# Kernel tuning notes

Hardware: AMD Instinct MI355X
Metric: run time of the kernel (lower is better)

## Reference

```python
import jax, jax.numpy as jnp
import numpy as np

B, T, N_EMBD, HEAD = 4, 2048, 1024, 128


def setup_inputs() -> dict:
    key = jax.random.key(0)
    ks = jax.random.split(key, 7)
    s = 1.0 / np.sqrt(N_EMBD)
    return {
        "X": jax.random.normal(ks[0], (B, T, N_EMBD), dtype=jnp.float32),
        "Wk": jax.random.normal(ks[1], (N_EMBD, HEAD), dtype=jnp.float32) * s,
        "bk": jax.random.normal(ks[2], (HEAD,), dtype=jnp.float32) * 0.02,
        "Wq": jax.random.normal(ks[3], (N_EMBD, HEAD), dtype=jnp.float32) * s,
        "bq": jax.random.normal(ks[4], (HEAD,), dtype=jnp.float32) * 0.02,
        "Wv": jax.random.normal(ks[5], (N_EMBD, HEAD), dtype=jnp.float32) * s,
        "bv": jax.random.normal(ks[6], (HEAD,), dtype=jnp.float32) * 0.02,
    }


def reference(X, Wk, bk, Wq, bq, Wv, bv):
    # X: [B, T, C] with C = n_embd
    C = X.shape[-1]
    k = X @ Wk + bk  # [B, T, H]
    q = X @ Wq + bq  # [B, T, H]
    # NOTE: original computes k @ q^T (not q @ k^T) and scales by n_embd**-0.5.
    wei = jnp.einsum("bth,bsh->bts", k, q) * (C ** -0.5)  # [B, T, T]
    # NOTE: original's masked_fill is not in-place and its result is discarded,
    # so NO causal mask is actually applied. Dropout is identity (eval).
    wei = jax.nn.softmax(wei, axis=-1)
    v = X @ Wv + bv  # [B, T, H]
    out = jnp.einsum("bts,bsh->bth", wei, v)  # [B, T, H]
    return out
```

## Files before the change

kernel.cpp:

```cpp
#include <hip/hip_runtime.h>
#include <hip/hip_bf16.h>

#define Bn 4
#define Tn 2048
#define Cn 1024
#define Hn 128
#define Mn (Bn*Tn)
#define SCHUNKS 8
#define SCHUNK  (Tn/SCHUNKS)

typedef _Float16 f16;
typedef __attribute__((ext_vector_type(4))) _Float16 f16x4;
typedef __attribute__((ext_vector_type(8))) _Float16 f16x8;
typedef __attribute__((ext_vector_type(4))) float f32x4;

__global__ void prep_w(const float* __restrict__ Wk, const float* __restrict__ Wq,
                       const float* __restrict__ Wv, f16* __restrict__ Wt) {
    const int w = blockIdx.y;
    const float* W = (w == 0) ? Wk : (w == 1) ? Wq : Wv;
    int idx = blockIdx.x * 256 + threadIdx.x;
    int c = idx >> 7;
    int h = idx & 127;
    Wt[w * (Cn * Hn) + h * Cn + c] = (f16)W[idx];
}

__global__ __launch_bounds__(512) void qkv_gemm(const float* __restrict__ X,
                                                const f16* __restrict__ Wt,
                                                const float* __restrict__ bk,
                                                const float* __restrict__ bq,
                                                const float* __restrict__ bv,
                                                f16* __restrict__ proj) {
    __shared__ __align__(16) f16 As[32 * 72];
    __shared__ __align__(16) f16 Bs[384 * 72];

    const int tid  = threadIdx.x;
    const int r0   = blockIdx.x * 32;
    const int lane = tid & 63, wid = tid >> 6;
    const int quad = lane >> 4, l16 = lane & 15;
    const int nbase = wid * 48;

    f32x4 acc[2][3] = {};

    for (int k0 = 0; k0 < Cn; k0 += 64) {
        {
            int row = tid >> 4, c4 = tid & 15;
            float4 x = *(const float4*)(X + (r0 + row) * Cn + k0 + c4 * 4);
            f16x4 v = { (f16)x.x, (f16)x.y, (f16)x.z, (f16)x.w };
            *(f16x4*)(&As[row * 72 + c4 * 4]) = v;
        }
        for (int i = 0; i < 6; i++) {
            int ci = tid + 512 * i;
            int row = ci >> 3, cc = ci & 7;
            *(f16x8*)(&Bs[row * 72 + cc * 8]) =
                *(const f16x8*)(Wt + row * Cn + k0 + cc * 8);
        }
        __syncthreads();
        for (int ks = 0; ks < 2; ks++) {
            int kk = ks * 32;
            f16x8 af[2], bf[3];
            for (int mt = 0; mt < 2; mt++)
                af[mt] = *(const f16x8*)(&As[(mt * 16 + l16) * 72 + kk + quad * 8]);
            for (int nt = 0; nt < 3; nt++)
                bf[nt] = *(const f16x8*)(&Bs[(nbase + nt * 16 + l16) * 72 + kk + quad * 8]);
            for (int mt = 0; mt < 2; mt++)
                for (int nt = 0; nt < 3; nt++)
                    acc[mt][nt] = __builtin_amdgcn_mfma_f32_16x16x32_f16(
                        af[mt], bf[nt], acc[mt][nt], 0, 0, 0);
        }
        __syncthreads();
    }

    for (int nt = 0; nt < 3; nt++) {
        int n0 = nbase + nt * 16;
        int wsel = n0 >> 7;
        int col = (n0 & 127) + l16;
        const float* bias = (wsel == 0) ? bk : (wsel == 1) ? bq : bv;
        float bval = bias[col];
        float scale = (wsel == 0) ? 0.03125f : 1.0f;
        f16* P = proj + wsel * (Mn * Hn);
        for (int mt = 0; mt < 2; mt++)
            for (int r = 0; r < 4; r++) {
                int m = r0 + mt * 16 + quad * 4 + r;
                P[m * Hn + col] = (f16)((acc[mt][nt][r] + bval) * scale);
            }
    }
}

__global__ __launch_bounds__(256) void vt_transpose(const f16* __restrict__ pv,
                                                    f16* __restrict__ vT) {
    __shared__ __align__(16) f16 T[64 * 72];
    const int tid = threadIdx.x;
    const int s0 = blockIdx.x * 64, h0 = blockIdx.y * 64, b = blockIdx.z;
    for (int i = 0; i < 2; i++) {
        int ci = tid + 256 * i;
        int row = ci >> 3, hc = ci & 7;
        *(f16x8*)(&T[row * 72 + hc * 8]) =
            *(const f16x8*)(pv + (b * Tn + s0 + row) * Hn + h0 + hc * 8);
    }
    __syncthreads();
    for (int i = 0; i < 2; i++) {
        int ci = tid + 256 * i;
        int h = ci >> 3, sc = ci & 7;
        f16x8 v;
        for (int j = 0; j < 8; j++) v[j] = T[(sc * 8 + j) * 72 + h];
        *(f16x8*)(&vT[(b * Hn + h0 + h) * Tn + s0 + sc * 8]) = v;
    }
}

__global__ __launch_bounds__(256, 2) void attn_kernel(const f16* __restrict__ pk,
                                                      const f16* __restrict__ pq,
                                                      const f16* __restrict__ vT,
                                                      f16* __restrict__ pO,
                                                      float* __restrict__ pm,
                                                      float* __restrict__ pl) {
    __shared__ __align__(16) char smem[36864];
    f16* Bq = (f16*)smem;
    f16* Vt = (f16*)(smem + 17408);

    const int tid  = threadIdx.x;
    const int tblk = blockIdx.x, c = blockIdx.y, b = blockIdx.z;
    const int t0   = tblk * 128;
    const int lane = tid & 63, wid = tid >> 6;
    const int quad = lane >> 4, l16 = lane & 15;
    const int tw   = t0 + wid * 32;

    const f16* kp = pk + b * Tn * Hn;
    const f16* qp = pq + b * Tn * Hn;
    const f16* vp = vT + b * Hn * Tn;

    f16x8 kfr[2][4];
    for (int tt = 0; tt < 2; tt++)
        for (int ks = 0; ks < 4; ks++)
            kfr[tt][ks] = *(const f16x8*)(kp + (tw + tt * 16 + l16) * Hn + ks * 32 + quad * 8);

    float m_i[2] = { -3e38f, -3e38f }, l_i[2] = { 0.0f, 0.0f };
    f32x4 accO[2][8] = {};

    for (int si = 0; si < SCHUNK / 64; si++) {
        const int s0 = c * SCHUNK + si * 64;
        for (int i = 0; i < 4; i++) {
            int ci = tid + 256 * i;
            int row = ci >> 4, hc = ci & 15;
            *(f16x8*)(&Bq[row * 136 + hc * 8]) =
                *(const f16x8*)(qp + (s0 + row) * Hn + hc * 8);
        }
        for (int i = 0; i < 4; i++) {
            int ci = tid + 256 * i;
            int h = ci >> 3, sc = ci & 7;
            *(f16x8*)(&Vt[h * 72 + sc * 8]) =
                *(const f16x8*)(vp + h * Tn + s0 + sc * 8);
        }
        __syncthreads();

        f32x4 accS[2][4] = {};
        for (int ks = 0; ks < 4; ks++) {
            int kk = ks * 32;
            for (int st = 0; st < 4; st++) {
                f16x8 af = *(const f16x8*)(&Bq[(st * 16 + l16) * 136 + kk + quad * 8]);
                accS[0][st] = __builtin_amdgcn_mfma_f32_16x16x32_f16(af, kfr[0][ks], accS[0][st], 0, 0, 0);
                accS[1][st] = __builtin_amdgcn_mfma_f32_16x16x32_f16(af, kfr[1][ks], accS[1][st], 0, 0, 0);
            }
        }

        f16x4 pf[2][4];
        for (int tt = 0; tt < 2; tt++) {
            float mloc = -3e38f;
            for (int st = 0; st < 4; st++)
                for (int r = 0; r < 4; r++) mloc = fmaxf(mloc, accS[tt][st][r]);
            mloc = fmaxf(mloc, __shfl_xor(mloc, 16));
            mloc = fmaxf(mloc, __shfl_xor(mloc, 32));
            float mnew = fmaxf(m_i[tt], mloc);
            float alpha = __expf(m_i[tt] - mnew);
            m_i[tt] = mnew;
            float psum = 0.0f;
            for (int st = 0; st < 4; st++) {
                f32x4 p;
                for (int r = 0; r < 4; r++) {
                    p[r] = __expf(accS[tt][st][r] - mnew);
                    psum += p[r];
                }
                pf[tt][st] = { (f16)p[0], (f16)p[1], (f16)p[2], (f16)p[3] };
            }
            psum += __shfl_xor(psum, 16);
            psum += __shfl_xor(psum, 32);
            l_i[tt] = l_i[tt] * alpha + psum;
            for (int ht = 0; ht < 8; ht++)
                for (int r = 0; r < 4; r++) accO[tt][ht][r] *= alpha;
        }

        for (int st = 0; st < 4; st++) {
            for (int ht = 0; ht < 8; ht++) {
                f16x4 av = *(const f16x4*)(&Vt[(ht * 16 + l16) * 72 + st * 16 + quad * 4]);
                accO[0][ht] = __builtin_amdgcn_mfma_f32_16x16x16f16(av, pf[0][st], accO[0][ht], 0, 0, 0);
                accO[1][ht] = __builtin_amdgcn_mfma_f32_16x16x16f16(av, pf[1][st], accO[1][ht], 0, 0, 0);
            }
        }
        __syncthreads();
    }

    for (int tt = 0; tt < 2; tt++) {
        __syncthreads();
        float* ep = (float*)smem + wid * 2048;
        for (int ht = 0; ht < 8; ht++)
            for (int r = 0; r < 4; r++)
                ep[(ht * 16 + quad * 4 + r) * 16 + l16] = accO[tt][ht][r];
        __syncthreads();
        {
            int t = lane >> 2, hq = lane & 3;
            int tgl = tw + tt * 16 + t;
            f16* dst = pO + ((size_t)(c * Bn + b) * Tn + tgl) * Hn + hq * 32;
            for (int g = 0; g < 4; g++) {
                f16x8 v;
                for (int j = 0; j < 8; j++)
                    v[j] = (f16)ep[(hq * 32 + g * 8 + j) * 16 + t];
                *(f16x8*)(dst + g * 8) = v;
            }
        }
        if (quad == 0) {
            pm[(c * Bn + b) * Tn + tw + tt * 16 + l16] = m_i[tt];
            pl[(c * Bn + b) * Tn + tw + tt * 16 + l16] = l_i[tt];
        }
    }
}

__global__ __launch_bounds__(256) void merge_kernel(const f16* __restrict__ pO,
                                                    const float* __restrict__ pm,
                                                    const float* __restrict__ pl,
                                                    float* __restrict__ out) {
    int gid = blockIdx.x * 256 + threadIdx.x;
    int tg = gid >> 2;
    int hq = gid & 3;
    float mc[SCHUNKS], lc[SCHUNKS];
    float M = -3e38f;
    for (int cI = 0; cI < SCHUNKS; cI++) {
        mc[cI] = pm[cI * (Bn * Tn) + tg];
        lc[cI] = pl[cI * (Bn * Tn) + tg];
        M = fmaxf(M, mc[cI]);
    }
    float L = 0.0f, wc[SCHUNKS];
    for (int cI = 0; cI < SCHUNKS; cI++) {
        wc[cI] = __expf(mc[cI] - M);
        L += wc[cI] * lc[cI];
    }
    float inv = 1.0f / L;
    float o[32] = {};
    for (int cI = 0; cI < SCHUNKS; cI++) {
        const f16* src = pO + ((size_t)cI * Bn * Tn + tg) * Hn + hq * 32;
        float w = wc[cI];
        for (int g = 0; g < 4; g++) {
            f16x8 v = *(const f16x8*)(src + g * 8);
            for (int j = 0; j < 8; j++) o[g * 8 + j] += w * (float)v[j];
        }
    }
    float* dst = out + (size_t)tg * Hn + hq * 32;
    for (int g = 0; g < 8; g++) {
        float4 v = { o[g*4+0] * inv, o[g*4+1] * inv, o[g*4+2] * inv, o[g*4+3] * inv };
        *(float4*)(dst + g * 4) = v;
    }
}

extern "C" void kernel_launch(void* const* d_in, const int* in_sizes, int n_in,
                              void* d_out, int out_size, void* d_ws, size_t ws_size,
                              hipStream_t stream) {
    const float* X  = (const float*)d_in[0];
    const float* Wk = (const float*)d_in[1];
    const float* bk = (const float*)d_in[2];
    const float* Wq = (const float*)d_in[3];
    const float* bq = (const float*)d_in[4];
    const float* Wv = (const float*)d_in[5];
    const float* bv = (const float*)d_in[6];
    float* out = (float*)d_out;

    char* base = (char*)d_ws;
    f16*   Wt   = (f16*)(base);
    f16*   proj = (f16*)(base + 786432);
    f16*   pk   = proj;
    f16*   pq   = proj + Mn * Hn;
    f16*   pv   = proj + 2 * Mn * Hn;
    f16*   vT   = (f16*)(base + 7077888);
    f16*   pO   = (f16*)(base + 9175040);
    float* pm   = (float*)(base + 25952256);
    float* pl   = (float*)(base + 26214400);

    prep_w<<<dim3(512, 3), 256, 0, stream>>>(Wk, Wq, Wv, Wt);
    qkv_gemm<<<dim3(Mn / 32), 512, 0, stream>>>(X, Wt, bk, bq, bv, proj);
    vt_transpose<<<dim3(Tn / 64, Hn / 64, Bn), 256, 0, stream>>>(pv, vT);
    attn_kernel<<<dim3(Tn / 128, SCHUNKS, Bn), 256, 0, stream>>>(pk, pq, vT, pO, pm, pl);
    merge_kernel<<<dim3(128), 256, 0, stream>>>(pO, pm, pl, out);
}
```

Before: 136.4 us.

## Fuse V transpose into QKV GEMM epilogue and prefetch Q/V tiles in attention

The QKV GEMM now uses 64-row tiles split across two column halves. It stages its output through shared memory so it can write K and Q directly and write V already transposed, which removes the separate vt_transpose kernel and its extra round trip through global memory. The attention kernel now loads the next Q/V chunk into registers while the current chunk is computed, a software prefetch that hides global load latency but raises register pressure. The GEMM retiling reads each X tile twice across the two column blocks and changes occupancy.

```diff
diff --git a/kernel.cpp b/kernel.cpp
--- a/kernel.cpp
+++ b/kernel.cpp
@@ -29,39 +29,44 @@
                                                 const float* __restrict__ bk,
                                                 const float* __restrict__ bq,
                                                 const float* __restrict__ bv,
-                                                f16* __restrict__ proj) {
-    __shared__ __align__(16) f16 As[32 * 72];
-    __shared__ __align__(16) f16 Bs[384 * 72];
+                                                f16* __restrict__ pk,
+                                                f16* __restrict__ pq,
+                                                f16* __restrict__ vT) {
+    __shared__ __align__(16) char smem[36864];
+    f16* As = (f16*)smem;
+    f16* Bs = (f16*)(smem + 9216);
 
     const int tid  = threadIdx.x;
-    const int r0   = blockIdx.x * 32;
+    const int r0   = blockIdx.x * 64;
+    const int ns   = blockIdx.y;
     const int lane = tid & 63, wid = tid >> 6;
     const int quad = lane >> 4, l16 = lane & 15;
-    const int nbase = wid * 48;
+    const int wm = wid >> 2, wn = wid & 3;
 
     f32x4 acc[2][3] = {};
 
     for (int k0 = 0; k0 < Cn; k0 += 64) {
-        {
-            int row = tid >> 4, c4 = tid & 15;
+        for (int i = 0; i < 2; i++) {
+            int ci = tid + 512 * i;
+            int row = ci >> 4, c4 = ci & 15;
             float4 x = *(const float4*)(X + (r0 + row) * Cn + k0 + c4 * 4);
             f16x4 v = { (f16)x.x, (f16)x.y, (f16)x.z, (f16)x.w };
             *(f16x4*)(&As[row * 72 + c4 * 4]) = v;
         }
-        for (int i = 0; i < 6; i++) {
+        for (int i = 0; i < 3; i++) {
             int ci = tid + 512 * i;
             int row = ci >> 3, cc = ci & 7;
             *(f16x8*)(&Bs[row * 72 + cc * 8]) =
-                *(const f16x8*)(Wt + row * Cn + k0 + cc * 8);
+                *(const f16x8*)(Wt + (ns * 192 + row) * Cn + k0 + cc * 8);
         }
         __syncthreads();
         for (int ks = 0; ks < 2; ks++) {
             int kk = ks * 32;
             f16x8 af[2], bf[3];
             for (int mt = 0; mt < 2; mt++)
-                af[mt] = *(const f16x8*)(&As[(mt * 16 + l16) * 72 + kk + quad * 8]);
+                af[mt] = *(const f16x8*)(&As[(wm * 32 + mt * 16 + l16) * 72 + kk + quad * 8]);
             for (int nt = 0; nt < 3; nt++)
-                bf[nt] = *(const f16x8*)(&Bs[(nbase + nt * 16 + l16) * 72 + kk + quad * 8]);
+                bf[nt] = *(const f16x8*)(&Bs[(wn * 48 + nt * 16 + l16) * 72 + kk + quad * 8]);
             for (int mt = 0; mt < 2; mt++)
                 for (int nt = 0; nt < 3; nt++)
                     acc[mt][nt] = __builtin_amdgcn_mfma_f32_16x16x32_f16(
@@ -70,40 +75,49 @@
         __syncthreads();
     }
 
+    f16* E = (f16*)smem;
     for (int nt = 0; nt < 3; nt++) {
-        int n0 = nbase + nt * 16;
+        int n0 = ns * 192 + wn * 48 + nt * 16;
         int wsel = n0 >> 7;
         int col = (n0 & 127) + l16;
         const float* bias = (wsel == 0) ? bk : (wsel == 1) ? bq : bv;
         float bval = bias[col];
         float scale = (wsel == 0) ? 0.03125f : 1.0f;
-        f16* P = proj + wsel * (Mn * Hn);
         for (int mt = 0; mt < 2; mt++)
             for (int r = 0; r < 4; r++) {
-                int m = r0 + mt * 16 + quad * 4 + r;
-                P[m * Hn + col] = (f16)((acc[mt][nt][r] + bval) * scale);
-            }
-    }
-}
-
-__global__ __launch_bounds__(256) void vt_transpose(const f16* __restrict__ pv,
-                                                    f16* __restrict__ vT) {
-    __shared__ __align__(16) f16 T[64 * 72];
-    const int tid = threadIdx.x;
-    const int s0 = blockIdx.x * 64, h0 = blockIdx.y * 64, b = blockIdx.z;
-    for (int i = 0; i < 2; i++) {
-        int ci = tid + 256 * i;
-        int row = ci >> 3, hc = ci & 7;
-        *(f16x8*)(&T[row * 72 + hc * 8]) =
-            *(const f16x8*)(pv + (b * Tn + s0 + row) * Hn + h0 + hc * 8);
+                int mrow = wm * 32 + mt * 16 + quad * 4 + r;
+                E[mrow * 200 + wn * 48 + nt * 16 + l16] =
+                    (f16)((acc[mt][nt][r] + bval) * scale);
+            }
     }
     __syncthreads();
-    for (int i = 0; i < 2; i++) {
-        int ci = tid + 256 * i;
-        int h = ci >> 3, sc = ci & 7;
-        f16x8 v;
-        for (int j = 0; j < 8; j++) v[j] = T[(sc * 8 + j) * 72 + h];
-        *(f16x8*)(&vT[(b * Hn + h0 + h) * Tn + s0 + sc * 8]) = v;
+
+    if (ns == 0) {
+        for (int i = 0; i < 3; i++) {
+            int ci = tid + 512 * i;
+            int row = ci / 24, c = ci % 24;
+            f16x8 v = *(const f16x8*)(&E[row * 200 + c * 8]);
+            int gn = c * 8;
+            f16* dst = (gn < 128) ? (pk + (r0 + row) * Hn + gn)
+                                  : (pq + (r0 + row) * Hn + (gn - 128));
+            *(f16x8*)dst = v;
+        }
+    } else {
+        {
+            int ci = tid;
+            int row = ci >> 3, c = ci & 7;
+            f16x8 v = *(const f16x8*)(&E[row * 200 + c * 8]);
+            *(f16x8*)(pq + (r0 + row) * Hn + 64 + c * 8) = v;
+        }
+        int b = r0 >> 11, sg = r0 & 2047;
+        for (int i = 0; i < 2; i++) {
+            int ci = tid + 512 * i;
+            int h = ci >> 3, sc = ci & 7;
+            f16x8 v;
+            for (int j = 0; j < 8; j++)
+                v[j] = E[(sc * 8 + j) * 200 + 64 + h];
+            *(f16x8*)(vT + (b * Hn + h) * Tn + sg + sc * 8) = v;
+        }
     }
 }
 
@@ -133,24 +147,38 @@
         for (int ks = 0; ks < 4; ks++)
             kfr[tt][ks] = *(const f16x8*)(kp + (tw + tt * 16 + l16) * Hn + ks * 32 + quad * 8);
 
+    const int qrow = tid >> 4 ;
+    (void)qrow;
+
     float m_i[2] = { -3e38f, -3e38f }, l_i[2] = { 0.0f, 0.0f };
     f32x4 accO[2][8] = {};
 
-    for (int si = 0; si < SCHUNK / 64; si++) {
-        const int s0 = c * SCHUNK + si * 64;
+    f16x8 qreg[4], vreg[4];
+    {
+        const int s0 = c * SCHUNK;
         for (int i = 0; i < 4; i++) {
             int ci = tid + 256 * i;
-            int row = ci >> 4, hc = ci & 15;
-            *(f16x8*)(&Bq[row * 136 + hc * 8]) =
-                *(const f16x8*)(qp + (s0 + row) * Hn + hc * 8);
-        }
+            qreg[i] = *(const f16x8*)(qp + (s0 + (ci >> 4)) * Hn + (ci & 15) * 8);
+            vreg[i] = *(const f16x8*)(vp + (ci >> 3) * Tn + s0 + (ci & 7) * 8);
+        }
+    }
+
+    for (int si = 0; si < SCHUNK / 64; si++) {
+        __syncthreads();
         for (int i = 0; i < 4; i++) {
             int ci = tid + 256 * i;
-            int h = ci >> 3, sc = ci & 7;
-            *(f16x8*)(&Vt[h * 72 + sc * 8]) =
-                *(const f16x8*)(vp + h * Tn + s0 + sc * 8);
-        }
-        __syncthreads();
+            *(f16x8*)(&Bq[(ci >> 4) * 136 + (ci & 15) * 8]) = qreg[i];
+            *(f16x8*)(&Vt[(ci >> 3) * 72 + (ci & 7) * 8]) = vreg[i];
+        }
+        __syncthreads();
+        if (si + 1 < SCHUNK / 64) {
+            const int s1 = c * SCHUNK + (si + 1) * 64;
+            for (int i = 0; i < 4; i++) {
+                int ci = tid + 256 * i;
+                qreg[i] = *(const f16x8*)(qp + (s1 + (ci >> 4)) * Hn + (ci & 15) * 8);
+                vreg[i] = *(const f16x8*)(vp + (ci >> 3) * Tn + s1 + (ci & 7) * 8);
+            }
+        }
 
         f32x4 accS[2][4] = {};
         for (int ks = 0; ks < 4; ks++) {
@@ -195,7 +223,6 @@
                 accO[1][ht] = __builtin_amdgcn_mfma_f32_16x16x16f16(av, pf[1][st], accO[1][ht], 0, 0, 0);
             }
         }
-        __syncthreads();
     }
 
     for (int tt = 0; tt < 2; tt++) {
@@ -272,19 +299,16 @@
     float* out = (float*)d_out;
 
     char* base = (char*)d_ws;
-    f16*   Wt   = (f16*)(base);
-    f16*   proj = (f16*)(base + 786432);
-    f16*   pk   = proj;
-    f16*   pq   = proj + Mn * Hn;
-    f16*   pv   = proj + 2 * Mn * Hn;
-    f16*   vT   = (f16*)(base + 7077888);
-    f16*   pO   = (f16*)(base + 9175040);
-    float* pm   = (float*)(base + 25952256);
-    float* pl   = (float*)(base + 26214400);
+    f16*   Wt = (f16*)(base);
+    f16*   pk = (f16*)(base + 786432);
+    f16*   pq = (f16*)(base + 2883584);
+    f16*   vT = (f16*)(base + 4980736);
+    f16*   pO = (f16*)(base + 7077888);
+    float* pm = (float*)(base + 23855104);
+    float* pl = (float*)(base + 24117248);
 
     prep_w<<<dim3(512, 3), 256, 0, stream>>>(Wk, Wq, Wv, Wt);
-    qkv_gemm<<<dim3(Mn / 32), 512, 0, stream>>>(X, Wt, bk, bq, bv, proj);
-    vt_transpose<<<dim3(Tn / 64, Hn / 64, Bn), 256, 0, stream>>>(pv, vT);
+    qkv_gemm<<<dim3(Mn / 64, 2), 512, 0, stream>>>(X, Wt, bk, bq, bv, pk, pq, vT);
     attn_kernel<<<dim3(Tn / 128, SCHUNKS, Bn), 256, 0, stream>>>(pk, pq, vT, pO, pm, pl);
     merge_kernel<<<dim3(128), 256, 0, stream>>>(pO, pm, pl, out);
 }
```

Result: faster. 131.0 us (-4.0%).
